# Performance work log

Measured on AMD Instinct MI355X. Metric: run time of the kernel, lower is better.

Reference implementation:

```python
import jax, jax.numpy as jnp
import numpy as np

N = 50000      # nodes
E = 800000     # edges (before self loops)
IN = 128       # in_channels
HID = 64       # hidden_channels
HEADS = 4      # num_heads
OUT = 40       # out_channels
NEG_SLOPE = 0.2


def setup_inputs() -> dict:
    key = jax.random.key(0)
    ks = jax.random.split(key, 16)
    x = jax.random.normal(ks[0], (N, IN), dtype=jnp.float32)
    edge_index = jax.random.randint(ks[1], (2, E), 0, N, dtype=jnp.int64)

    def lin(k, fan_in, fan_out):
        return jax.random.normal(k, (fan_in, fan_out), dtype=jnp.float32) * (1.0 / np.sqrt(fan_in))

    def att(k, h, c):
        return jax.random.normal(k, (h, c), dtype=jnp.float32) * (1.0 / np.sqrt(c))

    return {
        "x": x, "edge_index": edge_index,
        "W1": lin(ks[2], IN, HEADS * HID),
        "as1": att(ks[3], HEADS, HID), "ad1": att(ks[4], HEADS, HID),
        "b1": jnp.zeros((HEADS * HID,), jnp.float32),
        "W2": lin(ks[5], HEADS * HID, HEADS * HID),
        "as2": att(ks[6], HEADS, HID), "ad2": att(ks[7], HEADS, HID),
        "b2": jnp.zeros((HEADS * HID,), jnp.float32),
        "W3": lin(ks[8], HEADS * HID, OUT),
        "as3": att(ks[9], 1, OUT), "ad3": att(ks[10], 1, OUT),
        "b3": jnp.zeros((OUT,), jnp.float32),
    }


def _gat_layer(x, src, dst, W, a_src, a_dst, b):
    """One GATConv: linear -> per-edge attention -> segment softmax -> scatter-sum."""
    n = x.shape[0]
    H, C = a_src.shape
    h = (x @ W).reshape(n, H, C)                       # [N,H,C]
    al_s = jnp.einsum('nhc,hc->nh', h, a_src)          # [N,H]
    al_d = jnp.einsum('nhc,hc->nh', h, a_dst)          # [N,H]
    alpha = jax.nn.leaky_relu(al_s[src] + al_d[dst], NEG_SLOPE)  # [Etot,H]
    m = jax.ops.segment_max(alpha, dst, num_segments=n)          # stable softmax over incoming edges
    e = jnp.exp(alpha - m[dst])
    denom = jax.ops.segment_sum(e, dst, num_segments=n)
    attn = e / denom[dst]                              # [Etot,H]
    out = jax.ops.segment_sum(h[src] * attn[:, :, None], dst, num_segments=n)  # [N,H,C]
    return out.reshape(n, H * C) + b


def reference(x, edge_index, W1, as1, ad1, b1, W2, as2, ad2, b2, W3, as3, ad3, b3):
    # add self loops once (PyG GATConv default add_self_loops=True)
    loops = jnp.arange(N, dtype=edge_index.dtype)
    src = jnp.concatenate([edge_index[0], loops])
    dst = jnp.concatenate([edge_index[1], loops])

    h = _gat_layer(x, src, dst, W1, as1, ad1, b1)
    h = jax.nn.relu(h)                                 # dropout is identity in eval mode
    h = _gat_layer(h, src, dst, W2, as2, ad2, b2)
    h = jax.nn.relu(h)
    h = _gat_layer(h, src, dst, W3, as3, ad3, b3)      # final layer: 1 head
    return jax.nn.log_softmax(h, axis=-1)
```

## Files before the change

kernel.cpp:

```cpp
#include <hip/hip_runtime.h>
#include <math.h>

#define N_NODES 50000
#define N_EDGES 800000
#define ETOT    (N_EDGES + N_NODES)
#define EPAD_MAX 1200000
#define IN_CH   128
#define OUT_CH  40
#define NEG     0.2f
#define CAP     64

#define NPF   98
#define NFINE 512
#define FCAP  2400

typedef __attribute__((ext_vector_type(8))) short bf16x8;
typedef __attribute__((ext_vector_type(4))) float f32x4;
typedef __attribute__((ext_vector_type(2))) float f32x2;

__device__ inline unsigned short f2bf(float f) {
    unsigned int u = __float_as_uint(f);
    return (unsigned short)((u + 0x7FFFu + ((u >> 16) & 1u)) >> 16);
}
__device__ inline float bf2f(unsigned short u) {
    return __uint_as_float((unsigned int)u << 16);
}
__device__ inline float lrelu(float a) { return (a > 0.f) ? a : NEG * a; }

__global__ __launch_bounds__(256) void k_bkt(const int* __restrict__ ei,
                                             int* __restrict__ fcur,
                                             unsigned int* __restrict__ fbuf,
                                             const float* __restrict__ W1,
                                             const float* __restrict__ W2,
                                             const float* __restrict__ W3,
                                             unsigned short* __restrict__ Wt1,
                                             unsigned short* __restrict__ Wt2,
                                             unsigned short* __restrict__ Wt3) {
    if (blockIdx.x >= 256) {
        int i = (blockIdx.x - 256) * 256 + threadIdx.x;
        if (i < 32768) {
            int n = i >> 7, k = i & 127;
            Wt1[i] = f2bf(W1[(long)k * 256 + n]);
        } else if (i < 98304) {
            int j = i - 32768;
            int n = j >> 8, k = j & 255;
            Wt2[j] = f2bf(W2[(long)k * 256 + n]);
        } else if (i < 114688) {
            int j = i - 98304;
            int n = j >> 8, k = j & 255;
            Wt3[j] = (n < OUT_CH) ? f2bf(W3[(long)k * OUT_CH + n]) : (unsigned short)0;
        }
        return;
    }
    __shared__ int lcnt[NFINE], lbase[NFINE], lcur[NFINE];
    int tid = threadIdx.x;
    for (int i = tid; i < NFINE; i += 256) lcnt[i] = 0;
    __syncthreads();
    for (int i = blockIdx.x * 256 + tid; i < ETOT; i += 256 * 256) {
        int d = (i < N_EDGES) ? ei[N_EDGES + i] : (i - N_EDGES);
        atomicAdd(&lcnt[d / NPF], 1);
    }
    __syncthreads();
    for (int i = tid; i < NFINE; i += 256) {
        lbase[i] = atomicAdd(&fcur[i], lcnt[i]);
        lcur[i] = 0;
    }
    __syncthreads();
    for (int i = blockIdx.x * 256 + tid; i < ETOT; i += 256 * 256) {
        int s, d;
        if (i < N_EDGES) { s = ei[i]; d = ei[N_EDGES + i]; }
        else             { s = i - N_EDGES; d = s; }
        int p = d / NPF;
        int off = atomicAdd(&lcur[p], 1);
        fbuf[(long)p * FCAP + lbase[p] + off] = (unsigned int)s | ((unsigned int)d << 16);
    }
}

__global__ __launch_bounds__(256) void k_deg(const int* __restrict__ fcur,
                                             const unsigned int* __restrict__ fbuf,
                                             int* __restrict__ deg) {
    __shared__ int cnt[NPF];
    int f = blockIdx.x;
    int tid = threadIdx.x;
    int n0 = f * NPF;
    int nend = min(n0 + NPF, N_NODES);
    if (tid < NPF) cnt[tid] = 0;
    __syncthreads();
    int n = fcur[f];
    for (int i = tid; i < n; i += 256)
        atomicAdd(&cnt[(int)(fbuf[(long)f * FCAP + i] >> 16) - n0], 1);
    __syncthreads();
    if (tid < NPF && n0 + tid < nend) deg[n0 + tid] = cnt[tid];
}

__global__ void k_scan1(const int* __restrict__ deg, int* __restrict__ start,
                        int* __restrict__ bsum) {
    __shared__ int sh[256];
    int tid = threadIdx.x;
    int i = blockIdx.x * 256 + tid;
    int v = (i < N_NODES) ? ((deg[i] + 7) & ~7) : 0;
    int x = v;
    sh[tid] = x;
    __syncthreads();
    #pragma unroll
    for (int off = 1; off < 256; off <<= 1) {
        int t = (tid >= off) ? sh[tid - off] : 0;
        __syncthreads();
        x += t;
        sh[tid] = x;
        __syncthreads();
    }
    if (i < N_NODES) start[i] = x - v;
    if (tid == 255) bsum[blockIdx.x] = x;
}

__global__ void k_scan3(int* __restrict__ start, const int* __restrict__ bsum,
                        int nb) {
    __shared__ int sh[256];
    __shared__ int ex[256];
    int tid = threadIdx.x;
    int v = (tid < nb) ? bsum[tid] : 0;
    int x = v;
    sh[tid] = x;
    __syncthreads();
    #pragma unroll
    for (int off = 1; off < 256; off <<= 1) {
        int t = (tid >= off) ? sh[tid - off] : 0;
        __syncthreads();
        x += t;
        sh[tid] = x;
        __syncthreads();
    }
    ex[tid] = x - v;
    __syncthreads();
    int add = ex[blockIdx.x];
    int i = blockIdx.x * 256 + tid;
    if (i < N_NODES) start[i] += add;
}

__global__ __launch_bounds__(256) void k_scat(const int* __restrict__ fcur,
                                              const unsigned int* __restrict__ fbuf,
                                              const int* __restrict__ start,
                                              int* __restrict__ eSrc) {
    __shared__ int offs[NPF];
    __shared__ int base[NPF];
    int f = blockIdx.x;
    int tid = threadIdx.x;
    int n0 = f * NPF;
    int nend = min(n0 + NPF, N_NODES);
    int nn = nend - n0;
    if (tid < NPF && tid < nn) {
        int b = start[n0 + tid];
        offs[tid] = b;
        base[tid] = b;
    }
    __syncthreads();
    int n = fcur[f];
    for (int i = tid; i < n; i += 256) {
        unsigned int u = fbuf[(long)f * FCAP + i];
        int d = (int)(u >> 16);
        int pos = atomicAdd(&offs[d - n0], 1);
        eSrc[pos] = (int)(u & 0xFFFFu);
    }
    __syncthreads();
    if (tid < NPF && tid < nn) {
        int endp = offs[tid];
        int dg = endp - base[tid];
        int stop = base[tid] + ((dg + 7) & ~7);
        for (int k2 = endp; k2 < stop; ++k2) eSrc[k2] = -1;
    }
}

#define PITCH 40
template<int BN, int FM, int FN, bool CVT, bool FP8OUT, bool L4>
__global__ __launch_bounds__(256) void k_mfma(const void* __restrict__ Araw,
                                              const unsigned short* __restrict__ Bt,
                                              void* __restrict__ Cout,
                                              const float* __restrict__ a_s,
                                              const float* __restrict__ a_d,
                                              float* __restrict__ als,
                                              float* __restrict__ ald,
                                              int M, int K, int Ncol) {
    __shared__ unsigned short As[128 * PITCH];
    __shared__ unsigned short Bs[BN * PITCH];
    const int WCOLS = BN / (FN * 16);
    int tid = threadIdx.x;
    int wave = tid >> 6, lane = tid & 63;
    int quad = lane >> 4, l16 = lane & 15;
    int wr = wave / WCOLS, wc = wave % WCOLS;
    long row0 = (long)blockIdx.x * 128;
    int col0 = blockIdx.y * BN;

    f32x4 acc[FM][FN] = {};

    for (int k0 = 0; k0 < K; k0 += 32) {
        for (int c = tid; c < 512; c += 256) {
            int r = c >> 2, kp = (c & 3) << 3;
            long gr = row0 + r;
            if (CVT) {
                const float* A32 = (const float*)Araw;
                ushort4 lo = {0,0,0,0}, hi = {0,0,0,0};
                if (gr < M) {
                    float4 v0 = *(const float4*)(A32 + gr * K + k0 + kp);
                    float4 v1 = *(const float4*)(A32 + gr * K + k0 + kp + 4);
                    lo.x = f2bf(v0.x); lo.y = f2bf(v0.y); lo.z = f2bf(v0.z); lo.w = f2bf(v0.w);
                    hi.x = f2bf(v1.x); hi.y = f2bf(v1.y); hi.z = f2bf(v1.z); hi.w = f2bf(v1.w);
                }
                *(ushort4*)(As + r * PITCH + kp) = lo;
                *(ushort4*)(As + r * PITCH + kp + 4) = hi;
            } else {
                const unsigned short* A16 = (const unsigned short*)Araw;
                uint4 v = {0u, 0u, 0u, 0u};
                if (gr < M) v = *(const uint4*)(A16 + gr * K + k0 + kp);
                *(uint4*)(As + r * PITCH + kp) = v;
            }
        }
        for (int c = tid; c < BN * 4; c += 256) {
            int r = c >> 2, kp = (c & 3) << 3;
            uint4 v = *(const uint4*)(Bt + (long)(col0 + r) * K + k0 + kp);
            *(uint4*)(Bs + r * PITCH + kp) = v;
        }
        __syncthreads();
        bf16x8 af[FM], bfr[FN];
        #pragma unroll
        for (int i = 0; i < FM; ++i)
            af[i] = *(const bf16x8*)(As + (wr * FM * 16 + i * 16 + l16) * PITCH + quad * 8);
        #pragma unroll
        for (int j = 0; j < FN; ++j)
            bfr[j] = *(const bf16x8*)(Bs + (wc * FN * 16 + j * 16 + l16) * PITCH + quad * 8);
        #pragma unroll
        for (int i = 0; i < FM; ++i)
            #pragma unroll
            for (int j = 0; j < FN; ++j)
                acc[i][j] = __builtin_amdgcn_mfma_f32_16x16x32_bf16(af[i], bfr[j], acc[i][j], 0, 0, 0);
        __syncthreads();
    }

    {
        int head = L4 ? (blockIdx.y * WCOLS + wc) : 0;
        float as_v[FN], ad_v[FN];
        #pragma unroll
        for (int j = 0; j < FN; ++j) {
            int cidx = j * 16 + l16;
            if (L4) {
                as_v[j] = a_s[head * 64 + cidx];
                ad_v[j] = a_d[head * 64 + cidx];
            } else {
                as_v[j] = (cidx < OUT_CH) ? a_s[cidx] : 0.f;
                ad_v[j] = (cidx < OUT_CH) ? a_d[cidx] : 0.f;
            }
        }
        #pragma unroll
        for (int i = 0; i < FM; ++i) {
            #pragma unroll
            for (int v = 0; v < 4; ++v) {
                float ps = acc[i][0][v] * as_v[0] + acc[i][1][v] * as_v[1]
                         + acc[i][2][v] * as_v[2] + acc[i][3][v] * as_v[3];
                float pd = acc[i][0][v] * ad_v[0] + acc[i][1][v] * ad_v[1]
                         + acc[i][2][v] * ad_v[2] + acc[i][3][v] * ad_v[3];
                #pragma unroll
                for (int off = 1; off < 16; off <<= 1) {
                    ps += __shfl_xor(ps, off);
                    pd += __shfl_xor(pd, off);
                }
                if (l16 == 0) {
                    long row = row0 + wr * (FM * 16) + i * 16 + quad * 4 + v;
                    if (row < M) {
                        if (L4) { als[row * 4 + head] = ps; ald[row * 4 + head] = pd; }
                        else    { als[row] = ps; ald[row] = pd; }
                    }
                }
            }
        }
    }

    if (FP8OUT) {
        unsigned char* C8 = (unsigned char*)Cout;
        #pragma unroll
        for (int i = 0; i < FM; ++i) {
            #pragma unroll
            for (int v = 0; v < 4; ++v) {
                long row = row0 + wr * FM * 16 + i * 16 + quad * 4 + v;
                if (row < M) {
                    int p01 = __builtin_amdgcn_cvt_pk_fp8_f32(acc[i][0][v], acc[i][1][v], 0, false);
                    int p23 = __builtin_amdgcn_cvt_pk_fp8_f32(acc[i][2][v], acc[i][3][v], 0, false);
                    unsigned char* b = C8 + row * 256 + col0 + wc * (FN * 16) + l16;
                    b[0]  = (unsigned char)(p01 & 0xFF);
                    b[16] = (unsigned char)((p01 >> 8) & 0xFF);
                    b[32] = (unsigned char)(p23 & 0xFF);
                    b[48] = (unsigned char)((p23 >> 8) & 0xFF);
                }
            }
        }
    } else {
        unsigned short* C = (unsigned short*)Cout;
        #pragma unroll
        for (int i = 0; i < FM; ++i) {
            long rowb = row0 + wr * FM * 16 + i * 16 + quad * 4;
            #pragma unroll
            for (int j = 0; j < FN; ++j) {
                int col = col0 + wc * FN * 16 + j * 16 + l16;
                if (col < Ncol) {
                    #pragma unroll
                    for (int v = 0; v < 4; ++v) {
                        long r = rowb + v;
                        if (r < M) C[r * Ncol + col] = f2bf(acc[i][j][v]);
                    }
                }
            }
        }
    }
}

__global__ __launch_bounds__(256) void k_agg4(const unsigned char* __restrict__ h8,
                                              const int* __restrict__ start,
                                              const int* __restrict__ deg,
                                              const int* __restrict__ eSrc,
                                              const float* __restrict__ als,
                                              const float* __restrict__ ald,
                                              const float* __restrict__ bias,
                                              unsigned short* __restrict__ out) {
    __shared__ float wbuf[2][CAP * 4];
    __shared__ int   sbuf[2][CAP];
    __shared__ float red[2][32][9];
    int tid = threadIdx.x;
    int wave = tid >> 6;
    int nib = wave >> 1;
    int sub = wave & 1;
    int node = blockIdx.x * 2 + nib;
    int lane = tid & 63;

    int st = start[node];
    int dgp = (deg[node] + 7) & ~7;
    const int* ep = eSrc + st;
    int ncap = (dgp < CAP) ? dgp : CAP;
    int hc = ((ncap >> 1) + 7) & ~7;
    if (hc > ncap) hc = ncap;
    int lo = sub ? hc : 0;
    int hi = sub ? ncap : hc;

    int l16 = lane & 15, headw = lane >> 4;
    float aldd4 = ald[node * 4 + headw];
    for (int c = lo; c < hi; c += 16) {
        int slot = c + l16;
        bool ok = (slot < hi);
        int raw = ok ? ep[slot] : -1;
        int ss = (raw < 0) ? 0 : raw;
        float a = als[(long)ss * 4 + headw] + aldd4;
        float w = (raw < 0) ? 0.f : __expf(lrelu(a));
        if (ok) {
            wbuf[nib][slot * 4 + headw] = w;
            if (headw == 0) sbuf[nib][slot] = ss;
        }
    }

    int half = lane >> 5;
    int hl = lane & 31;
    int head8 = hl >> 3;
    float den = 0.f;
    f32x2 acc2[4] = {};

    int pairs = (hi - lo) >> 1;
    for (int pi = 0; pi < pairs; pi += 4) {
        int s[4];
        float w[4];
        #pragma unroll
        for (int u = 0; u < 4; ++u) {
            int slot = lo + (pi + u) * 2 + half;
            s[u] = sbuf[nib][slot];
            w[u] = wbuf[nib][slot * 4 + head8];
        }
        uint2 hv[4];
        #pragma unroll
        for (int u = 0; u < 4; ++u)
            hv[u] = *(const uint2*)(h8 + (long)s[u] * 256 + hl * 8);
        #pragma unroll
        for (int u = 0; u < 4; ++u) {
            den += w[u];
            f32x2 w2; w2.x = w[u]; w2.y = w[u];
            acc2[0] += w2 * __builtin_amdgcn_cvt_pk_f32_fp8((int)hv[u].x, false);
            acc2[1] += w2 * __builtin_amdgcn_cvt_pk_f32_fp8((int)hv[u].x, true);
            acc2[2] += w2 * __builtin_amdgcn_cvt_pk_f32_fp8((int)hv[u].y, false);
            acc2[3] += w2 * __builtin_amdgcn_cvt_pk_f32_fp8((int)hv[u].y, true);
        }
    }

    if (sub == 1 && dgp > ncap) {
        float aldd8 = ald[node * 4 + head8];
        for (int j = ncap; j < dgp; j += 2) {
            int raw = ep[j + half];
            int ss = (raw < 0) ? 0 : raw;
            float w = (raw < 0) ? 0.f : __expf(lrelu(als[(long)ss * 4 + head8] + aldd8));
            uint2 hv = *(const uint2*)(h8 + (long)ss * 256 + hl * 8);
            den += w;
            f32x2 w2; w2.x = w; w2.y = w;
            acc2[0] += w2 * __builtin_amdgcn_cvt_pk_f32_fp8((int)hv.x, false);
            acc2[1] += w2 * __builtin_amdgcn_cvt_pk_f32_fp8((int)hv.x, true);
            acc2[2] += w2 * __builtin_amdgcn_cvt_pk_f32_fp8((int)hv.y, false);
            acc2[3] += w2 * __builtin_amdgcn_cvt_pk_f32_fp8((int)hv.y, true);
        }
    }

    den += __shfl_xor(den, 32);
    #pragma unroll
    for (int c = 0; c < 4; ++c) {
        acc2[c].x += __shfl_xor(acc2[c].x, 32);
        acc2[c].y += __shfl_xor(acc2[c].y, 32);
    }

    if (sub == 1 && half == 0) {
        #pragma unroll
        for (int c = 0; c < 4; ++c) {
            red[nib][hl][c * 2]     = acc2[c].x;
            red[nib][hl][c * 2 + 1] = acc2[c].y;
        }
        red[nib][hl][8] = den;
    }
    __syncthreads();
    if (sub == 0 && half == 0) {
        #pragma unroll
        for (int c = 0; c < 4; ++c) {
            acc2[c].x += red[nib][hl][c * 2];
            acc2[c].y += red[nib][hl][c * 2 + 1];
        }
        den += red[nib][hl][8];

        float inv = 1.f / den;
        int cb = hl * 8;
        float4 b0 = *(const float4*)(bias + cb);
        float4 b1 = *(const float4*)(bias + cb + 4);
        float v0 = fmaxf(acc2[0].x * inv + b0.x, 0.f);
        float v1 = fmaxf(acc2[0].y * inv + b0.y, 0.f);
        float v2 = fmaxf(acc2[1].x * inv + b0.z, 0.f);
        float v3 = fmaxf(acc2[1].y * inv + b0.w, 0.f);
        float v4 = fmaxf(acc2[2].x * inv + b1.x, 0.f);
        float v5 = fmaxf(acc2[2].y * inv + b1.y, 0.f);
        float v6 = fmaxf(acc2[3].x * inv + b1.z, 0.f);
        float v7 = fmaxf(acc2[3].y * inv + b1.w, 0.f);
        uint4 o;
        o.x = (unsigned int)f2bf(v0) | ((unsigned int)f2bf(v1) << 16);
        o.y = (unsigned int)f2bf(v2) | ((unsigned int)f2bf(v3) << 16);
        o.z = (unsigned int)f2bf(v4) | ((unsigned int)f2bf(v5) << 16);
        o.w = (unsigned int)f2bf(v6) | ((unsigned int)f2bf(v7) << 16);
        *(uint4*)(out + (long)node * 256 + cb) = o;
    }
}

__global__ __launch_bounds__(256) void k_agg1(const unsigned short* __restrict__ h,
                                              const int* __restrict__ start,
                                              const int* __restrict__ deg,
                                              const int* __restrict__ eSrc,
                                              const float* __restrict__ als,
                                              const float* __restrict__ ald,
                                              const float* __restrict__ bias,
                                              float* __restrict__ out) {
    int node = (blockIdx.x * blockDim.x + threadIdx.x) >> 6;
    int lane = threadIdx.x & 63;
    if (node >= N_NODES) return;
    int q = lane >> 4, r = lane & 15;
    bool act = (r < 10);
    int st = start[node];
    int dgp = (deg[node] + 7) & ~7;
    const int* ep = eSrc + st;
    float aldd = ald[node];

    float den = 0.f;
    float4 acc = {0.f, 0.f, 0.f, 0.f};

    int j = 0;
    for (; j + 16 <= dgp; j += 16) {
        int base = j + q * 4;
        int s[4];
        float w[4];
        #pragma unroll
        for (int u = 0; u < 4; ++u) s[u] = ep[base + u];
        #pragma unroll
        for (int u = 0; u < 4; ++u) {
            int raw = s[u];
            int ss = (raw < 0) ? 0 : raw;
            w[u] = (raw < 0) ? 0.f : __expf(lrelu(als[ss] + aldd));
            s[u] = ss;
        }
        ushort4 hh[4];
        #pragma unroll
        for (int u = 0; u < 4; ++u) {
            ushort4 t = {0, 0, 0, 0};
            if (act) t = *(const ushort4*)(h + (long)s[u] * OUT_CH + r * 4);
            hh[u] = t;
        }
        #pragma unroll
        for (int u = 0; u < 4; ++u) {
            den += w[u];
            acc.x += w[u] * bf2f(hh[u].x);
            acc.y += w[u] * bf2f(hh[u].y);
            acc.z += w[u] * bf2f(hh[u].z);
            acc.w += w[u] * bf2f(hh[u].w);
        }
    }
    if (j < dgp) {
        int base = j + q * 2;
        int s[2];
        float w[2];
        #pragma unroll
        for (int u = 0; u < 2; ++u) s[u] = ep[base + u];
        #pragma unroll
        for (int u = 0; u < 2; ++u) {
            int raw = s[u];
            int ss = (raw < 0) ? 0 : raw;
            w[u] = (raw < 0) ? 0.f : __expf(lrelu(als[ss] + aldd));
            s[u] = ss;
        }
        ushort4 hh[2];
        #pragma unroll
        for (int u = 0; u < 2; ++u) {
            ushort4 t = {0, 0, 0, 0};
            if (act) t = *(const ushort4*)(h + (long)s[u] * OUT_CH + r * 4);
            hh[u] = t;
        }
        #pragma unroll
        for (int u = 0; u < 2; ++u) {
            den += w[u];
            acc.x += w[u] * bf2f(hh[u].x);
            acc.y += w[u] * bf2f(hh[u].y);
            acc.z += w[u] * bf2f(hh[u].z);
            acc.w += w[u] * bf2f(hh[u].w);
        }
    }

    #pragma unroll
    for (int off = 16; off < 64; off <<= 1) {
        acc.x += __shfl_xor(acc.x, off);
        acc.y += __shfl_xor(acc.y, off);
        acc.z += __shfl_xor(acc.z, off);
        acc.w += __shfl_xor(acc.w, off);
        den   += __shfl_xor(den, off);
    }
    float inv = 1.f / den;
    float4 bv = {0.f, 0.f, 0.f, 0.f};
    if (act) bv = *(const float4*)(bias + r * 4);
    float4 v;
    v.x = acc.x * inv + bv.x;
    v.y = acc.y * inv + bv.y;
    v.z = acc.z * inv + bv.z;
    v.w = acc.w * inv + bv.w;
    float mx = act ? fmaxf(fmaxf(v.x, v.y), fmaxf(v.z, v.w)) : -INFINITY;
    #pragma unroll
    for (int off = 1; off < 16; off <<= 1) mx = fmaxf(mx, __shfl_xor(mx, off));
    float sum = act ? (__expf(v.x - mx) + __expf(v.y - mx) + __expf(v.z - mx) + __expf(v.w - mx)) : 0.f;
    #pragma unroll
    for (int off = 1; off < 16; off <<= 1) sum += __shfl_xor(sum, off);
    float lse = mx + logf(sum);
    if (q == 0 && act) {
        float4 o;
        o.x = v.x - lse;
        o.y = v.y - lse;
        o.z = v.z - lse;
        o.w = v.w - lse;
        *(float4*)(out + (long)node * OUT_CH + r * 4) = o;
    }
}

extern "C" void kernel_launch(void* const* d_in, const int* in_sizes, int n_in,
                              void* d_out, int out_size, void* d_ws, size_t ws_size,
                              hipStream_t stream) {
    (void)in_sizes; (void)n_in; (void)out_size; (void)ws_size;
    const float* x   = (const float*)d_in[0];
    const int*   ei  = (const int*)d_in[1];
    const float* W1  = (const float*)d_in[2];
    const float* as1 = (const float*)d_in[3];
    const float* ad1 = (const float*)d_in[4];
    const float* b1  = (const float*)d_in[5];
    const float* W2  = (const float*)d_in[6];
    const float* as2 = (const float*)d_in[7];
    const float* ad2 = (const float*)d_in[8];
    const float* b2  = (const float*)d_in[9];
    const float* W3  = (const float*)d_in[10];
    const float* as3 = (const float*)d_in[11];
    const float* ad3 = (const float*)d_in[12];
    const float* b3  = (const float*)d_in[13];
    float* out = (float*)d_out;

    char* p = (char*)d_ws;
    auto alloc = [&](size_t b) { char* r = p; p += (b + 255) & ~(size_t)255; return r; };
    int*   deg   = (int*)alloc((size_t)N_NODES * 4);
    int*   start = (int*)alloc((size_t)N_NODES * 4);
    int*   bsum  = (int*)alloc(256 * 4);
    int*   fcur  = (int*)alloc((size_t)NFINE * 4);
    unsigned int* fbuf = (unsigned int*)alloc((size_t)NFINE * FCAP * 4);
    int*   eSrc  = (int*)alloc((size_t)EPAD_MAX * 4);
    float* als   = (float*)alloc((size_t)N_NODES * 4 * 4);
    float* ald   = (float*)alloc((size_t)N_NODES * 4 * 4);
    unsigned char*  hA8  = (unsigned char*)alloc((size_t)N_NODES * 256);
    unsigned short* hBbf = (unsigned short*)alloc((size_t)N_NODES * 256 * 2);
    unsigned short* h3bf = (unsigned short*)alloc((size_t)N_NODES * OUT_CH * 2);
    unsigned short* Wt1  = (unsigned short*)alloc((size_t)256 * IN_CH * 2);
    unsigned short* Wt2  = (unsigned short*)alloc((size_t)256 * 256 * 2);
    unsigned short* Wt3  = (unsigned short*)alloc((size_t)64 * 256 * 2);

    const int NB = (N_NODES + 255) / 256;
    const int WB = (N_NODES + 3) / 4;
    const int AB = N_NODES / 2;
    const int MB = (N_NODES + 127) / 128;

    hipMemsetAsync(fcur, 0, (size_t)NFINE * 4, stream);
    k_bkt<<<256 + 448, 256, 0, stream>>>(ei, fcur, fbuf, W1, W2, W3, Wt1, Wt2, Wt3);
    k_deg<<<NFINE, 256, 0, stream>>>(fcur, fbuf, deg);
    k_scan1<<<NB, 256, 0, stream>>>(deg, start, bsum);
    k_scan3<<<NB, 256, 0, stream>>>(start, bsum, NB);
    k_scat<<<NFINE, 256, 0, stream>>>(fcur, fbuf, start, eSrc);

    k_mfma<128, 4, 4, true, true, true><<<dim3(MB, 2), 256, 0, stream>>>(
        x, Wt1, hA8, as1, ad1, als, ald, N_NODES, IN_CH, 256);
    k_agg4<<<AB, 256, 0, stream>>>(hA8, start, deg, eSrc, als, ald, b1, hBbf);

    k_mfma<128, 4, 4, false, true, true><<<dim3(MB, 2), 256, 0, stream>>>(
        hBbf, Wt2, hA8, as2, ad2, als, ald, N_NODES, 256, 256);
    k_agg4<<<AB, 256, 0, stream>>>(hA8, start, deg, eSrc, als, ald, b2, hBbf);

    k_mfma<64, 2, 4, false, false, false><<<dim3(MB, 1), 256, 0, stream>>>(
        hBbf, Wt3, h3bf, as3, ad3, als, ald, N_NODES, 256, OUT_CH);
    k_agg1<<<WB, 256, 0, stream>>>(h3bf, start, deg, eSrc, als, ald, b3, out);
}
```

Baseline: 322.0 us.

## Fuse CSR prefix scan into bucket kernels and use one wave per node in aggregation

```diff
diff --git a/kernel.cpp b/kernel.cpp
--- a/kernel.cpp
+++ b/kernel.cpp
@@ -78,70 +78,55 @@
 
 __global__ __launch_bounds__(256) void k_deg(const int* __restrict__ fcur,
                                              const unsigned int* __restrict__ fbuf,
-                                             int* __restrict__ deg) {
+                                             int* __restrict__ deg,
+                                             int* __restrict__ psum) {
     __shared__ int cnt[NPF];
+    __shared__ int tot;
     int f = blockIdx.x;
     int tid = threadIdx.x;
     int n0 = f * NPF;
     int nend = min(n0 + NPF, N_NODES);
+    int nn = nend - n0;
     if (tid < NPF) cnt[tid] = 0;
+    if (tid == 0) tot = 0;
     __syncthreads();
     int n = fcur[f];
     for (int i = tid; i < n; i += 256)
         atomicAdd(&cnt[(int)(fbuf[(long)f * FCAP + i] >> 16) - n0], 1);
     __syncthreads();
-    if (tid < NPF && n0 + tid < nend) deg[n0 + tid] = cnt[tid];
-}
-
-__global__ void k_scan1(const int* __restrict__ deg, int* __restrict__ start,
-                        int* __restrict__ bsum) {
-    __shared__ int sh[256];
+    if (tid < NPF && tid < nn) {
+        deg[n0 + tid] = cnt[tid];
+        atomicAdd(&tot, (cnt[tid] + 7) & ~7);
+    }
+    __syncthreads();
+    if (tid == 0) psum[f] = tot;
+}
+
+__global__ __launch_bounds__(512) void k_pscan(int* __restrict__ psum) {
+    __shared__ int sh[NFINE];
     int tid = threadIdx.x;
-    int i = blockIdx.x * 256 + tid;
-    int v = (i < N_NODES) ? ((deg[i] + 7) & ~7) : 0;
+    int v = psum[tid];
     int x = v;
     sh[tid] = x;
     __syncthreads();
     #pragma unroll
-    for (int off = 1; off < 256; off <<= 1) {
+    for (int off = 1; off < NFINE; off <<= 1) {
         int t = (tid >= off) ? sh[tid - off] : 0;
         __syncthreads();
         x += t;
         sh[tid] = x;
         __syncthreads();
     }
-    if (i < N_NODES) start[i] = x - v;
-    if (tid == 255) bsum[blockIdx.x] = x;
-}
-
-__global__ void k_scan3(int* __restrict__ start, const int* __restrict__ bsum,
-                        int nb) {
-    __shared__ int sh[256];
-    __shared__ int ex[256];
-    int tid = threadIdx.x;
-    int v = (tid < nb) ? bsum[tid] : 0;
-    int x = v;
-    sh[tid] = x;
-    __syncthreads();
-    #pragma unroll
-    for (int off = 1; off < 256; off <<= 1) {
-        int t = (tid >= off) ? sh[tid - off] : 0;
-        __syncthreads();
-        x += t;
-        sh[tid] = x;
-        __syncthreads();
-    }
-    ex[tid] = x - v;
-    __syncthreads();
-    int add = ex[blockIdx.x];
-    int i = blockIdx.x * 256 + tid;
-    if (i < N_NODES) start[i] += add;
+    psum[tid] = x - v;
 }
 
 __global__ __launch_bounds__(256) void k_scat(const int* __restrict__ fcur,
                                               const unsigned int* __restrict__ fbuf,
-                                              const int* __restrict__ start,
+                                              const int* __restrict__ deg,
+                                              const int* __restrict__ psum,
+                                              int* __restrict__ start,
                                               int* __restrict__ eSrc) {
+    __shared__ int sval[128];
     __shared__ int offs[NPF];
     __shared__ int base[NPF];
     int f = blockIdx.x;
@@ -149,12 +134,30 @@
     int n0 = f * NPF;
     int nend = min(n0 + NPF, N_NODES);
     int nn = nend - n0;
-    if (tid < NPF && tid < nn) {
-        int b = start[n0 + tid];
-        offs[tid] = b;
-        base[tid] = b;
-    }
-    __syncthreads();
+    int pbase = psum[f];
+
+    int pd = 0;
+    if (tid < 128) {
+        pd = (tid < nn) ? ((deg[n0 + tid] + 7) & ~7) : 0;
+        sval[tid] = pd;
+    }
+    __syncthreads();
+    #pragma unroll
+    for (int off = 1; off < 128; off <<= 1) {
+        int t = 0;
+        if (tid < 128 && tid >= off) t = sval[tid - off];
+        __syncthreads();
+        if (tid < 128) sval[tid] += t;
+        __syncthreads();
+    }
+    if (tid < 128 && tid < nn) {
+        int st = pbase + sval[tid] - pd;
+        start[n0 + tid] = st;
+        offs[tid] = st;
+        base[tid] = st;
+    }
+    __syncthreads();
+
     int n = fcur[f];
     for (int i = tid; i < n; i += 256) {
         unsigned int u = fbuf[(long)f * FCAP + i];
@@ -320,37 +323,29 @@
                                               const float* __restrict__ ald,
                                               const float* __restrict__ bias,
                                               unsigned short* __restrict__ out) {
-    __shared__ float wbuf[2][CAP * 4];
-    __shared__ int   sbuf[2][CAP];
-    __shared__ float red[2][32][9];
-    int tid = threadIdx.x;
-    int wave = tid >> 6;
-    int nib = wave >> 1;
-    int sub = wave & 1;
-    int node = blockIdx.x * 2 + nib;
-    int lane = tid & 63;
-
+    __shared__ float wbuf[4][CAP * 4];
+    __shared__ int   sbuf[4][CAP];
+    int wid = threadIdx.x >> 6;
+    int node = (blockIdx.x * blockDim.x + threadIdx.x) >> 6;
+    int lane = threadIdx.x & 63;
+    if (node >= N_NODES) return;
     int st = start[node];
     int dgp = (deg[node] + 7) & ~7;
     const int* ep = eSrc + st;
-    int ncap = (dgp < CAP) ? dgp : CAP;
-    int hc = ((ncap >> 1) + 7) & ~7;
-    if (hc > ncap) hc = ncap;
-    int lo = sub ? hc : 0;
-    int hi = sub ? ncap : hc;
 
     int l16 = lane & 15, headw = lane >> 4;
     float aldd4 = ald[node * 4 + headw];
-    for (int c = lo; c < hi; c += 16) {
+    int ncap = (dgp < CAP) ? dgp : CAP;
+    for (int c = 0; c < ncap; c += 16) {
         int slot = c + l16;
-        bool ok = (slot < hi);
+        bool ok = (slot < ncap);
         int raw = ok ? ep[slot] : -1;
         int ss = (raw < 0) ? 0 : raw;
         float a = als[(long)ss * 4 + headw] + aldd4;
         float w = (raw < 0) ? 0.f : __expf(lrelu(a));
         if (ok) {
-            wbuf[nib][slot * 4 + headw] = w;
-            if (headw == 0) sbuf[nib][slot] = ss;
+            wbuf[wid][slot * 4 + headw] = w;
+            if (headw == 0) sbuf[wid][slot] = ss;
         }
     }
 
@@ -360,15 +355,17 @@
     float den = 0.f;
     f32x2 acc2[4] = {};
 
-    int pairs = (hi - lo) >> 1;
-    for (int pi = 0; pi < pairs; pi += 4) {
+    int ncpair = ncap >> 1;
+    int jA = 0, jB = ncpair - 4;
+
+    auto do_pairs = [&](int p0, int p1, int p2, int p3) {
+        int slot[4] = {p0 * 2 + half, p1 * 2 + half, p2 * 2 + half, p3 * 2 + half};
         int s[4];
         float w[4];
         #pragma unroll
         for (int u = 0; u < 4; ++u) {
-            int slot = lo + (pi + u) * 2 + half;
-            s[u] = sbuf[nib][slot];
-            w[u] = wbuf[nib][slot * 4 + head8];
+            s[u] = sbuf[wid][slot[u]];
+            w[u] = wbuf[wid][slot[u] * 4 + head8];
         }
         uint2 hv[4];
         #pragma unroll
@@ -383,9 +380,19 @@
             acc2[2] += w2 * __builtin_amdgcn_cvt_pk_f32_fp8((int)hv[u].y, false);
             acc2[3] += w2 * __builtin_amdgcn_cvt_pk_f32_fp8((int)hv[u].y, true);
         }
-    }
-
-    if (sub == 1 && dgp > ncap) {
+    };
+
+    while (jA < jB) {
+        do_pairs(jA, jA + 1, jB, jB + 1);
+        do_pairs(jA + 2, jA + 3, jB + 2, jB + 3);
+        jA += 8; jB -= 8;
+        jA -= 4; jB += 4;
+    }
+    if (jA == jB) {
+        do_pairs(jA, jA + 1, jA + 2, jA + 3);
+    }
+
+    if (dgp > ncap) {
         float aldd8 = ald[node * 4 + head8];
         for (int j = ncap; j < dgp; j += 2) {
             int raw = ep[j + half];
@@ -408,23 +415,7 @@
         acc2[c].y += __shfl_xor(acc2[c].y, 32);
     }
 
-    if (sub == 1 && half == 0) {
-        #pragma unroll
-        for (int c = 0; c < 4; ++c) {
-            red[nib][hl][c * 2]     = acc2[c].x;
-            red[nib][hl][c * 2 + 1] = acc2[c].y;
-        }
-        red[nib][hl][8] = den;
-    }
-    __syncthreads();
-    if (sub == 0 && half == 0) {
-        #pragma unroll
-        for (int c = 0; c < 4; ++c) {
-            acc2[c].x += red[nib][hl][c * 2];
-            acc2[c].y += red[nib][hl][c * 2 + 1];
-        }
-        den += red[nib][hl][8];
-
+    if (half == 0) {
         float inv = 1.f / den;
         int cb = hl * 8;
         float4 b0 = *(const float4*)(bias + cb);
@@ -584,7 +575,7 @@
     auto alloc = [&](size_t b) { char* r = p; p += (b + 255) & ~(size_t)255; return r; };
     int*   deg   = (int*)alloc((size_t)N_NODES * 4);
     int*   start = (int*)alloc((size_t)N_NODES * 4);
-    int*   bsum  = (int*)alloc(256 * 4);
+    int*   psum  = (int*)alloc((size_t)NFINE * 4);
     int*   fcur  = (int*)alloc((size_t)NFINE * 4);
     unsigned int* fbuf = (unsigned int*)alloc((size_t)NFINE * FCAP * 4);
     int*   eSrc  = (int*)alloc((size_t)EPAD_MAX * 4);
@@ -597,25 +588,22 @@
     unsigned short* Wt2  = (unsigned short*)alloc((size_t)256 * 256 * 2);
     unsigned short* Wt3  = (unsigned short*)alloc((size_t)64 * 256 * 2);
 
-    const int NB = (N_NODES + 255) / 256;
     const int WB = (N_NODES + 3) / 4;
-    const int AB = N_NODES / 2;
     const int MB = (N_NODES + 127) / 128;
 
     hipMemsetAsync(fcur, 0, (size_t)NFINE * 4, stream);
     k_bkt<<<256 + 448, 256, 0, stream>>>(ei, fcur, fbuf, W1, W2, W3, Wt1, Wt2, Wt3);
-    k_deg<<<NFINE, 256, 0, stream>>>(fcur, fbuf, deg);
-    k_scan1<<<NB, 256, 0, stream>>>(deg, start, bsum);
-    k_scan3<<<NB, 256, 0, stream>>>(start, bsum, NB);
-    k_scat<<<NFINE, 256, 0, stream>>>(fcur, fbuf, start, eSrc);
+    k_deg<<<NFINE, 256, 0, stream>>>(fcur, fbuf, deg, psum);
+    k_pscan<<<1, NFINE, 0, stream>>>(psum);
+    k_scat<<<NFINE, 256, 0, stream>>>(fcur, fbuf, deg, psum, start, eSrc);
 
     k_mfma<128, 4, 4, true, true, true><<<dim3(MB, 2), 256, 0, stream>>>(
         x, Wt1, hA8, as1, ad1, als, ald, N_NODES, IN_CH, 256);
-    k_agg4<<<AB, 256, 0, stream>>>(hA8, start, deg, eSrc, als, ald, b1, hBbf);
+    k_agg4<<<WB, 256, 0, stream>>>(hA8, start, deg, eSrc, als, ald, b1, hBbf);
 
     k_mfma<128, 4, 4, false, true, true><<<dim3(MB, 2), 256, 0, stream>>>(
         hBbf, Wt2, hA8, as2, ad2, als, ald, N_NODES, 256, 256);
-    k_agg4<<<AB, 256, 0, stream>>>(hA8, start, deg, eSrc, als, ald, b2, hBbf);
+    k_agg4<<<WB, 256, 0, stream>>>(hA8, start, deg, eSrc, als, ald, b2, hBbf);
 
     k_mfma<64, 2, 4, false, false, false><<<dim3(MB, 1), 256, 0, stream>>>(
         hBbf, Wt3, h3bf, as3, ad3, als, ald, N_NODES, 256, OUT_CH);
```

New measurement: 317.1 us. No clear change (-1.5%).
